# Optimization experiments

Hardware: AMD Instinct MI355X
Metric: run time of the kernel (lower is better)

## Reference

```python
import jax, jax.numpy as jnp
import numpy as np

N = 4096      # number of nodes
C = 8         # channels (w1..w8 in source)
IN_DIM = 256  # input feature dim
D = 64        # per-channel dim (c_dim)
OUT = 128     # out_dim
ITERS = 4     # routing iterations
BETA = 1.0    # temperature
DENSITY = 0.01


def _l2norm(x):
    # tf.nn.l2_normalize along last axis with eps=1e-12
    return x * jax.lax.rsqrt(jnp.maximum(jnp.sum(x * x, axis=-1, keepdims=True), 1e-12))


def setup_inputs() -> dict:
    key = jax.random.key(0)
    k0, k1, k2, k3, k4, k5 = jax.random.split(key, 6)
    features = jax.random.normal(k0, (N, IN_DIM), dtype=jnp.float32)
    # sparse-ish 0/1 adjacency stored densely (as in the original model)
    adj = (jax.random.uniform(k1, (N, N)) < DENSITY).astype(jnp.float32)
    W = jax.random.normal(k2, (C, IN_DIM, D), dtype=jnp.float32)    # w1..w8 stacked
    b = jax.random.normal(k3, (C, 1, D), dtype=jnp.float32)         # b1..b8 stacked
    W_o = jax.random.normal(k4, (C * D, OUT), dtype=jnp.float32)
    bias = jax.random.normal(k5, (1, OUT), dtype=jnp.float32)
    return {"features": features, "adj": adj, "W": W, "b": b, "W_o": W_o, "bias": bias}


def reference(features, adj, W, b, W_o, bias):
    mask = adj > 0  # [N, N]
    # per-channel projection + l2 normalize: z[c] = l2norm(features @ w[c] + b[c])
    z = _l2norm(jnp.einsum('ni,cid->cnd', features, W) + b)  # [C, N, D]
    for _ in range(ITERS):
        # dense per-channel attention (XX^T), masked by adjacency
        A = jnp.einsum('cnd,cmd->cnm', z, z)                 # [C, N, N]
        A = jnp.where(mask[None], A, 0.0) / BETA
        # softmax across channels at each (i, j), then re-mask
        A = jax.nn.softmax(A, axis=0)
        A = jnp.where(mask[None], A, 0.0)
        # aggregate + residual + l2 normalize
        z = _l2norm(z + jnp.einsum('cnm,cmd->cnd', A, z))
    # concat channels along feature axis: [N, C*D]
    h = jnp.transpose(z, (1, 0, 2)).reshape(N, C * D)
    # (dropout skipped: stochastic op, identity in the deterministic reference)
    return h @ W_o + bias
```

## Files before the change

kernel.cpp:

```cpp
#include <hip/hip_runtime.h>
#include <hip/hip_bf16.h>

#define N_NODES 4096
#define C_CH    8
#define IN_DIM  256
#define D_DIM   64
#define CD      512
#define OUT_DIM 128
#define ITERS   4
#define STRIDE  128

typedef __hip_bfloat16 bf16;
typedef short short8 __attribute__((ext_vector_type(8)));
typedef float floatx4 __attribute__((ext_vector_type(4)));

__device__ __forceinline__ float bf2f(bf16 x) { return __bfloat162float(x); }

__device__ __forceinline__ unsigned f2b_rne(float x) {
    unsigned u = __float_as_uint(x);
    return (u + 0x7FFFu + ((u >> 16) & 1u)) >> 16;
}
__device__ __forceinline__ unsigned pack2bf(float a, float b) {
    return f2b_rne(a) | (f2b_rne(b) << 16);
}
__device__ __forceinline__ void unpack2(unsigned v, float& a, float& b) {
    a = __uint_as_float(v << 16);
    b = __uint_as_float(v & 0xFFFF0000u);
}
__device__ __forceinline__ short8 as_s8(uint4 u) {
    union { uint4 a; short8 b; } x; x.a = u; return x.b;
}

__global__ void detect_kernel(const unsigned* __restrict__ feat_u,
                              int* __restrict__ flag) {
    int t = threadIdx.x;
    unsigned u = feat_u[t];
    int e = (u >> 7) & 0xFF;
    int vote = (e >= 0x68 && e <= 0x86) ? 1 : 0;
    __shared__ int sv[4];
    int lane = t & 63, wid = t >> 6;
    #pragma unroll
    for (int off = 32; off; off >>= 1) vote += __shfl_xor(vote, off);
    if (lane == 0) sv[wid] = vote;
    __syncthreads();
    if (t == 0) flag[0] = (sv[0] + sv[1] + sv[2] + sv[3] >= 128) ? 1 : 0;
}

__global__ void wflat_kernel(const void* __restrict__ W, float* __restrict__ Wflat,
                             const int* __restrict__ flag) {
    int idx = blockIdx.x * 256 + threadIdx.x;
    int d = idx & 63;
    int k = (idx >> 6) & 255;
    int c = idx >> 14;
    float v = (*flag) ? bf2f(((const bf16*)W)[idx]) : ((const float*)W)[idx];
    Wflat[k * CD + c * D_DIM + d] = v;
}

__global__ void wot_kernel(const void* __restrict__ Wo,
                           unsigned short* __restrict__ Wo_t,
                           const int* __restrict__ flag) {
    int idx = blockIdx.x * 256 + threadIdx.x;
    int k = idx >> 7, n = idx & 127;
    unsigned short v;
    if (*flag) v = ((const unsigned short*)Wo)[idx];
    else       v = (unsigned short)f2b_rne(((const float*)Wo)[idx]);
    Wo_t[n * CD + k] = v;
}

__global__ __launch_bounds__(256) void proj_kernel(
        const void* __restrict__ feat, const float* __restrict__ Wflat,
        const void* __restrict__ b, unsigned* __restrict__ zbf,
        const int* __restrict__ flag) {
    int nb = blockIdx.x * 8;
    int t  = threadIdx.x;
    __shared__ float fs[8 * IN_DIM];
    bool isbf = (*flag) != 0;

    if (isbf) {
        const uint4* p = (const uint4*)((const unsigned short*)feat + (size_t)nb * IN_DIM);
        uint4 u = p[t];
        float v[8];
        unpack2(u.x, v[0], v[1]); unpack2(u.y, v[2], v[3]);
        unpack2(u.z, v[4], v[5]); unpack2(u.w, v[6], v[7]);
        *(float4*)&fs[t * 8]     = make_float4(v[0], v[1], v[2], v[3]);
        *(float4*)&fs[t * 8 + 4] = make_float4(v[4], v[5], v[6], v[7]);
    } else {
        const float4* p = (const float4*)((const float*)feat + (size_t)nb * IN_DIM);
        float4 u0 = p[t];
        float4 u1 = p[t + 256];
        *(float4*)&fs[t * 4]         = u0;
        *(float4*)&fs[(t + 256) * 4] = u1;
    }
    __syncthreads();

    float a0[8] = {}, a1[8] = {};
    for (int k = 0; k < IN_DIM; k++) {
        float w0 = Wflat[k * CD + t];
        float w1 = Wflat[k * CD + 256 + t];
        #pragma unroll
        for (int r = 0; r < 8; r++) {
            float f = fs[r * IN_DIM + k];
            a0[r] = fmaf(f, w0, a0[r]);
            a1[r] = fmaf(f, w1, a1[r]);
        }
    }
    float b0 = isbf ? bf2f(((const bf16*)b)[t])       : ((const float*)b)[t];
    float b1 = isbf ? bf2f(((const bf16*)b)[256 + t]) : ((const float*)b)[256 + t];

    #pragma unroll
    for (int r = 0; r < 8; r++) {
        float v0 = a0[r] + b0;
        float v1 = a1[r] + b1;
        float ss0 = v0 * v0, ss1 = v1 * v1;
        #pragma unroll
        for (int off = 32; off; off >>= 1) {
            ss0 += __shfl_xor(ss0, off);
            ss1 += __shfl_xor(ss1, off);
        }
        float o0 = v0 * rsqrtf(fmaxf(ss0, 1e-12f));
        float o1 = v1 * rsqrtf(fmaxf(ss1, 1e-12f));
        size_t row = (size_t)(nb + r);
        float p0 = __shfl_xor(o0, 1);
        float p1 = __shfl_xor(o1, 1);
        if (!(t & 1)) {
            zbf[row * 256 + (t >> 1)]       = pack2bf(o0, p0);
            zbf[row * 256 + 128 + (t >> 1)] = pack2bf(o1, p1);
        }
    }
}

__global__ __launch_bounds__(256) void build_kernel(
        const void* __restrict__ adj, int* __restrict__ deg,
        int* __restrict__ col_buf, const int* __restrict__ flag) {
    int w = threadIdx.x >> 6, lane = threadIdx.x & 63;
    int i = blockIdx.x * 4 + w;
    bool isbf = (*flag) != 0;
    int base_out = i * STRIDE;
    int running = 0;
    int nch = isbf ? 8 : 16;

    for (int ch = 0; ch < nch; ch++) {
        unsigned bits = 0;
        int j0, nelem;
        if (isbf) {
            const uint4* p = (const uint4*)((const unsigned short*)adj + (size_t)i * N_NODES);
            uint4 u = p[ch * 64 + lane];
            j0 = (ch * 64 + lane) * 8; nelem = 8;
            unsigned short h[8] = {
                (unsigned short)(u.x & 0xFFFF), (unsigned short)(u.x >> 16),
                (unsigned short)(u.y & 0xFFFF), (unsigned short)(u.y >> 16),
                (unsigned short)(u.z & 0xFFFF), (unsigned short)(u.z >> 16),
                (unsigned short)(u.w & 0xFFFF), (unsigned short)(u.w >> 16)};
            #pragma unroll
            for (int k = 0; k < 8; k++)
                if ((h[k] & 0x8000) == 0 && h[k] != 0) bits |= (1u << k);
        } else {
            const float4* p = (const float4*)((const float*)adj + (size_t)i * N_NODES);
            float4 f = p[ch * 64 + lane];
            j0 = (ch * 64 + lane) * 4; nelem = 4;
            if (f.x > 0.f) bits |= 1u;
            if (f.y > 0.f) bits |= 2u;
            if (f.z > 0.f) bits |= 4u;
            if (f.w > 0.f) bits |= 8u;
        }
        int cnt = __popc(bits);
        int sc = cnt;
        #pragma unroll
        for (int off = 1; off < 64; off <<= 1) {
            int v = __shfl_up(sc, off);
            if (lane >= off) sc += v;
        }
        int tot = __shfl(sc, 63);
        int pos = base_out + running + (sc - cnt);
        for (int k = 0; k < nelem; k++) {
            if ((bits >> k) & 1u) {
                if (pos < base_out + STRIDE) col_buf[pos] = j0 + k;
                pos++;
            }
        }
        running += tot;
    }
    if (lane == 0) deg[i] = (running < STRIDE) ? running : STRIDE;
}

__device__ __forceinline__ void edge_step(const float zi[8], float acc[8], uint4 u) {
    float vj[8];
    unpack2(u.x, vj[0], vj[1]);
    unpack2(u.y, vj[2], vj[3]);
    unpack2(u.z, vj[4], vj[5]);
    unpack2(u.w, vj[6], vj[7]);
    float p = 0.f;
    #pragma unroll
    for (int k = 0; k < 8; k++) p = fmaf(zi[k], vj[k], p);
    p += __shfl_xor(p, 1); p += __shfl_xor(p, 2); p += __shfl_xor(p, 4);
    float ex = __expf(p);
    float s = ex;
    s += __shfl_xor(s, 8); s += __shfl_xor(s, 16); s += __shfl_xor(s, 32);
    float wgt = ex / s;
    #pragma unroll
    for (int k = 0; k < 8; k++) acc[k] = fmaf(wgt, vj[k], acc[k]);
}

__global__ __launch_bounds__(256) void route_kernel(
        const unsigned* __restrict__ zbf_in, unsigned* __restrict__ zbf_out,
        const int* __restrict__ deg, const int* __restrict__ col_buf) {
    int w = threadIdx.x >> 6, lane = threadIdx.x & 63;
    int pair = w >> 1;
    int half = w & 1;
    int i = blockIdx.x * 2 + pair;
    int g = lane >> 3, s = lane & 7;
    __shared__ int   s_cols[2][STRIDE];
    __shared__ float s_acc[2][CD];

    s_cols[pair][half * 64 + lane] = col_buf[i * STRIDE + half * 64 + lane];
    __syncthreads();

    int frag = g * 32 + s * 4;
    uint4 uown = *(const uint4*)(zbf_in + (size_t)i * 256 + frag);
    float zi[8], acc[8];
    unpack2(uown.x, zi[0], zi[1]); unpack2(uown.y, zi[2], zi[3]);
    unpack2(uown.z, zi[4], zi[5]); unpack2(uown.w, zi[6], zi[7]);
    #pragma unroll
    for (int k = 0; k < 8; k++) acc[k] = half ? 0.f : zi[k];

    int dg = deg[i];
    int e_mid = (dg + 1) >> 1;
    int e   = half ? e_mid : 0;
    int end = half ? dg    : e_mid;
    for (; e + 3 < end; e += 4) {
        int j0 = s_cols[pair][e]     & (N_NODES - 1);
        int j1 = s_cols[pair][e + 1] & (N_NODES - 1);
        int j2 = s_cols[pair][e + 2] & (N_NODES - 1);
        int j3 = s_cols[pair][e + 3] & (N_NODES - 1);
        uint4 u0 = *(const uint4*)(zbf_in + (size_t)j0 * 256 + frag);
        uint4 u1 = *(const uint4*)(zbf_in + (size_t)j1 * 256 + frag);
        uint4 u2 = *(const uint4*)(zbf_in + (size_t)j2 * 256 + frag);
        uint4 u3 = *(const uint4*)(zbf_in + (size_t)j3 * 256 + frag);
        edge_step(zi, acc, u0);
        edge_step(zi, acc, u1);
        edge_step(zi, acc, u2);
        edge_step(zi, acc, u3);
    }
    for (; e < end; e++) {
        int j0 = s_cols[pair][e] & (N_NODES - 1);
        uint4 u0 = *(const uint4*)(zbf_in + (size_t)j0 * 256 + frag);
        edge_step(zi, acc, u0);
    }

    int flat = g * D_DIM + s * 8;
    if (half) {
        *(float4*)&s_acc[pair][flat]     = make_float4(acc[0], acc[1], acc[2], acc[3]);
        *(float4*)&s_acc[pair][flat + 4] = make_float4(acc[4], acc[5], acc[6], acc[7]);
    }
    __syncthreads();
    if (!half) {
        float4 p0 = *(const float4*)&s_acc[pair][flat];
        float4 p1 = *(const float4*)&s_acc[pair][flat + 4];
        acc[0] += p0.x; acc[1] += p0.y; acc[2] += p0.z; acc[3] += p0.w;
        acc[4] += p1.x; acc[5] += p1.y; acc[6] += p1.z; acc[7] += p1.w;

        float ss = 0.f;
        #pragma unroll
        for (int k = 0; k < 8; k++) ss = fmaf(acc[k], acc[k], ss);
        ss += __shfl_xor(ss, 1); ss += __shfl_xor(ss, 2); ss += __shfl_xor(ss, 4);
        float sc = rsqrtf(fmaxf(ss, 1e-12f));
        float o[8];
        #pragma unroll
        for (int k = 0; k < 8; k++) o[k] = acc[k] * sc;

        uint4 ob;
        ob.x = pack2bf(o[0], o[1]); ob.y = pack2bf(o[2], o[3]);
        ob.z = pack2bf(o[4], o[5]); ob.w = pack2bf(o[6], o[7]);
        *(uint4*)(zbf_out + (size_t)i * 256 + frag) = ob;
    }
}

__global__ __launch_bounds__(256) void out_gemm_mfma(
        const unsigned* __restrict__ zbf, const unsigned* __restrict__ wot_u,
        const void* __restrict__ bias, void* __restrict__ out,
        const int* __restrict__ flag) {
    int w = threadIdx.x >> 6, lane = threadIdx.x & 63;
    int r0 = blockIdx.x * 32 + (w & 1) * 16;
    int n0 = (w >> 1) * 64;
    int m = lane & 15, quad = lane >> 4;

    floatx4 acc0 = {0.f, 0.f, 0.f, 0.f}, acc1 = acc0, acc2 = acc0, acc3 = acc0;
    const unsigned* ap  = zbf   + (size_t)(r0 + m) * 256 + quad * 4;
    const unsigned* bp0 = wot_u + (size_t)(n0 + m) * 256 + quad * 4;
    const unsigned* bp1 = bp0 + 16 * 256;
    const unsigned* bp2 = bp0 + 32 * 256;
    const unsigned* bp3 = bp0 + 48 * 256;

    #pragma unroll
    for (int k0 = 0; k0 < 256; k0 += 16) {
        short8 a  = as_s8(*(const uint4*)(ap  + k0));
        short8 b0 = as_s8(*(const uint4*)(bp0 + k0));
        short8 b1 = as_s8(*(const uint4*)(bp1 + k0));
        short8 b2 = as_s8(*(const uint4*)(bp2 + k0));
        short8 b3 = as_s8(*(const uint4*)(bp3 + k0));
        acc0 = __builtin_amdgcn_mfma_f32_16x16x32_bf16(a, b0, acc0, 0, 0, 0);
        acc1 = __builtin_amdgcn_mfma_f32_16x16x32_bf16(a, b1, acc1, 0, 0, 0);
        acc2 = __builtin_amdgcn_mfma_f32_16x16x32_bf16(a, b2, acc2, 0, 0, 0);
        acc3 = __builtin_amdgcn_mfma_f32_16x16x32_bf16(a, b3, acc3, 0, 0, 0);
    }

    bool isbf = (*flag) != 0;
    float accs[4][4] = {
        {acc0[0], acc0[1], acc0[2], acc0[3]},
        {acc1[0], acc1[1], acc1[2], acc1[3]},
        {acc2[0], acc2[1], acc2[2], acc2[3]},
        {acc3[0], acc3[1], acc3[2], acc3[3]}};
    #pragma unroll
    for (int c = 0; c < 4; c++) {
        int col = n0 + c * 16 + m;
        float bb = isbf ? bf2f(((const bf16*)bias)[col]) : ((const float*)bias)[col];
        #pragma unroll
        for (int r = 0; r < 4; r++) {
            int row = r0 + quad * 4 + r;
            float v = accs[c][r] + bb;
            size_t oi = (size_t)row * OUT_DIM + col;
            if (isbf) ((bf16*)out)[oi] = __float2bfloat16(v);
            else      ((float*)out)[oi] = v;
        }
    }
}

extern "C" void kernel_launch(void* const* d_in, const int* in_sizes, int n_in,
                              void* d_out, int out_size, void* d_ws, size_t ws_size,
                              hipStream_t stream) {
    const void* feat = d_in[0];
    const void* adj  = d_in[1];
    const void* W    = d_in[2];
    const void* b    = d_in[3];
    const void* Wo   = d_in[4];
    const void* bias = d_in[5];

    char* ws = (char*)d_ws;
    unsigned*       zbf_a = (unsigned*)ws;
    unsigned*       zbf_b = (unsigned*)(ws + (4u  << 20));
    unsigned short* Wo_t  = (unsigned short*)(ws + (8u << 20));
    float*          Wflat = (float*)(ws + (9u << 20));
    int*            flag  = (int*)  (ws + (10u << 20));
    int*            deg   = (int*)  (ws + (10u << 20) + (4u << 10));
    int*            col_buf = (int*)(ws + (11u << 20));

    detect_kernel<<<1, 256, 0, stream>>>((const unsigned*)feat, flag);
    wflat_kernel<<<(C_CH * IN_DIM * D_DIM) / 256, 256, 0, stream>>>(W, Wflat, flag);
    wot_kernel<<<(CD * OUT_DIM) / 256, 256, 0, stream>>>(Wo, Wo_t, flag);
    build_kernel<<<N_NODES / 4, 256, 0, stream>>>(adj, deg, col_buf, flag);
    proj_kernel<<<N_NODES / 8, 256, 0, stream>>>(feat, Wflat, b, zbf_a, flag);

    unsigned* bin = zbf_a;
    unsigned* bot = zbf_b;
    for (int it = 0; it < ITERS; it++) {
        route_kernel<<<N_NODES / 2, 256, 0, stream>>>(bin, bot, deg, col_buf);
        unsigned* tb = bin; bin = bot; bot = tb;
    }
    out_gemm_mfma<<<N_NODES / 32, 256, 0, stream>>>(bin, (const unsigned*)Wo_t, bias, d_out, flag);
}
```

Before: 248.7 us.

## Fuse preprocessing kernels and run routing iterations in one cooperative kernel

Merges the dtype detection, W flattening, Wo transpose, adjacency compaction and projection into a single heterogeneous launch, with each block inferring the dtype itself. The four routing iterations run in one cooperative kernel that separates them with grid-wide syncs, using one wave per node instead of splitting a node across two waves. The projection now reads W directly in its original layout instead of a pre-flattened copy, and the divide and rsqrt become fast hardware rcp/rsq. The aim is to cut launch overhead and the extra pass that materialised Wflat. In exchange, each wave walks the full edge list alone, so there is less parallelism per node, and grid sync has its own cost.

```diff
diff --git a/kernel.cpp b/kernel.cpp
--- a/kernel.cpp
+++ b/kernel.cpp
@@ -1,5 +1,8 @@
 #include <hip/hip_runtime.h>
 #include <hip/hip_bf16.h>
+#include <hip/hip_cooperative_groups.h>
+
+namespace cg = cooperative_groups;
 
 #define N_NODES 4096
 #define C_CH    8
@@ -31,156 +34,146 @@
     union { uint4 a; short8 b; } x; x.a = u; return x.b;
 }
 
-__global__ void detect_kernel(const unsigned* __restrict__ feat_u,
-                              int* __restrict__ flag) {
-    int t = threadIdx.x;
-    unsigned u = feat_u[t];
+__device__ __forceinline__ bool wave_detect(const unsigned* __restrict__ feat_u) {
+    int lane = threadIdx.x & 63;
+    unsigned u = feat_u[lane];
     int e = (u >> 7) & 0xFF;
     int vote = (e >= 0x68 && e <= 0x86) ? 1 : 0;
-    __shared__ int sv[4];
-    int lane = t & 63, wid = t >> 6;
     #pragma unroll
     for (int off = 32; off; off >>= 1) vote += __shfl_xor(vote, off);
-    if (lane == 0) sv[wid] = vote;
-    __syncthreads();
-    if (t == 0) flag[0] = (sv[0] + sv[1] + sv[2] + sv[3] >= 128) ? 1 : 0;
-}
-
-__global__ void wflat_kernel(const void* __restrict__ W, float* __restrict__ Wflat,
-                             const int* __restrict__ flag) {
-    int idx = blockIdx.x * 256 + threadIdx.x;
-    int d = idx & 63;
-    int k = (idx >> 6) & 255;
-    int c = idx >> 14;
-    float v = (*flag) ? bf2f(((const bf16*)W)[idx]) : ((const float*)W)[idx];
-    Wflat[k * CD + c * D_DIM + d] = v;
-}
-
-__global__ void wot_kernel(const void* __restrict__ Wo,
-                           unsigned short* __restrict__ Wo_t,
-                           const int* __restrict__ flag) {
-    int idx = blockIdx.x * 256 + threadIdx.x;
-    int k = idx >> 7, n = idx & 127;
-    unsigned short v;
-    if (*flag) v = ((const unsigned short*)Wo)[idx];
-    else       v = (unsigned short)f2b_rne(((const float*)Wo)[idx]);
-    Wo_t[n * CD + k] = v;
-}
-
-__global__ __launch_bounds__(256) void proj_kernel(
-        const void* __restrict__ feat, const float* __restrict__ Wflat,
-        const void* __restrict__ b, unsigned* __restrict__ zbf,
-        const int* __restrict__ flag) {
-    int nb = blockIdx.x * 8;
-    int t  = threadIdx.x;
-    __shared__ float fs[8 * IN_DIM];
-    bool isbf = (*flag) != 0;
-
-    if (isbf) {
-        const uint4* p = (const uint4*)((const unsigned short*)feat + (size_t)nb * IN_DIM);
-        uint4 u = p[t];
-        float v[8];
-        unpack2(u.x, v[0], v[1]); unpack2(u.y, v[2], v[3]);
-        unpack2(u.z, v[4], v[5]); unpack2(u.w, v[6], v[7]);
-        *(float4*)&fs[t * 8]     = make_float4(v[0], v[1], v[2], v[3]);
-        *(float4*)&fs[t * 8 + 4] = make_float4(v[4], v[5], v[6], v[7]);
+    return vote >= 32;
+}
+
+__global__ __launch_bounds__(256) void mega_pre(
+        const void* __restrict__ feat, const void* __restrict__ adj,
+        const void* __restrict__ W, const void* __restrict__ b,
+        const void* __restrict__ Wo,
+        unsigned* __restrict__ zbf, int* __restrict__ deg,
+        int* __restrict__ col_buf, unsigned short* __restrict__ Wo_t) {
+    bool isbf = wave_detect((const unsigned*)feat);
+    int bx = blockIdx.x;
+    int t = threadIdx.x;
+
+    if (bx < 512) {
+        int nb = bx * 8;
+        __shared__ float fs[8 * IN_DIM];
+        if (isbf) {
+            const uint4* p = (const uint4*)((const unsigned short*)feat + (size_t)nb * IN_DIM);
+            uint4 u = p[t];
+            float v[8];
+            unpack2(u.x, v[0], v[1]); unpack2(u.y, v[2], v[3]);
+            unpack2(u.z, v[4], v[5]); unpack2(u.w, v[6], v[7]);
+            *(float4*)&fs[t * 8]     = make_float4(v[0], v[1], v[2], v[3]);
+            *(float4*)&fs[t * 8 + 4] = make_float4(v[4], v[5], v[6], v[7]);
+        } else {
+            const float4* p = (const float4*)((const float*)feat + (size_t)nb * IN_DIM);
+            float4 u0 = p[t];
+            float4 u1 = p[t + 256];
+            *(float4*)&fs[t * 4]         = u0;
+            *(float4*)&fs[(t + 256) * 4] = u1;
+        }
+        __syncthreads();
+
+        int d = t & 63;
+        size_t wbase0 = (size_t)(t >> 6) * IN_DIM * D_DIM + d;
+        size_t wbase1 = (size_t)(4 + (t >> 6)) * IN_DIM * D_DIM + d;
+        float a0[8] = {}, a1[8] = {};
+        for (int k = 0; k < IN_DIM; k++) {
+            float w0, w1;
+            if (isbf) {
+                w0 = bf2f(((const bf16*)W)[wbase0 + k * D_DIM]);
+                w1 = bf2f(((const bf16*)W)[wbase1 + k * D_DIM]);
+            } else {
+                w0 = ((const float*)W)[wbase0 + k * D_DIM];
+                w1 = ((const float*)W)[wbase1 + k * D_DIM];
+            }
+            #pragma unroll
+            for (int r = 0; r < 8; r++) {
+                float f = fs[r * IN_DIM + k];
+                a0[r] = fmaf(f, w0, a0[r]);
+                a1[r] = fmaf(f, w1, a1[r]);
+            }
+        }
+        float b0 = isbf ? bf2f(((const bf16*)b)[t])       : ((const float*)b)[t];
+        float b1 = isbf ? bf2f(((const bf16*)b)[256 + t]) : ((const float*)b)[256 + t];
+
+        #pragma unroll
+        for (int r = 0; r < 8; r++) {
+            float v0 = a0[r] + b0;
+            float v1 = a1[r] + b1;
+            float ss0 = v0 * v0, ss1 = v1 * v1;
+            #pragma unroll
+            for (int off = 32; off; off >>= 1) {
+                ss0 += __shfl_xor(ss0, off);
+                ss1 += __shfl_xor(ss1, off);
+            }
+            float o0 = v0 * __builtin_amdgcn_rsqf(fmaxf(ss0, 1e-12f));
+            float o1 = v1 * __builtin_amdgcn_rsqf(fmaxf(ss1, 1e-12f));
+            size_t row = (size_t)(nb + r);
+            float p0 = __shfl_xor(o0, 1);
+            float p1 = __shfl_xor(o1, 1);
+            if (!(t & 1)) {
+                zbf[row * 256 + (t >> 1)]       = pack2bf(o0, p0);
+                zbf[row * 256 + 128 + (t >> 1)] = pack2bf(o1, p1);
+            }
+        }
+    } else if (bx < 1536) {
+        int w = t >> 6, lane = t & 63;
+        int i = (bx - 512) * 4 + w;
+        int base_out = i * STRIDE;
+        int running = 0;
+        int nch = isbf ? 8 : 16;
+        for (int ch = 0; ch < nch; ch++) {
+            unsigned bits = 0;
+            int j0, nelem;
+            if (isbf) {
+                const uint4* p = (const uint4*)((const unsigned short*)adj + (size_t)i * N_NODES);
+                uint4 u = p[ch * 64 + lane];
+                j0 = (ch * 64 + lane) * 8; nelem = 8;
+                unsigned short h[8] = {
+                    (unsigned short)(u.x & 0xFFFF), (unsigned short)(u.x >> 16),
+                    (unsigned short)(u.y & 0xFFFF), (unsigned short)(u.y >> 16),
+                    (unsigned short)(u.z & 0xFFFF), (unsigned short)(u.z >> 16),
+                    (unsigned short)(u.w & 0xFFFF), (unsigned short)(u.w >> 16)};
+                #pragma unroll
+                for (int k = 0; k < 8; k++)
+                    if ((h[k] & 0x8000) == 0 && h[k] != 0) bits |= (1u << k);
+            } else {
+                const float4* p = (const float4*)((const float*)adj + (size_t)i * N_NODES);
+                float4 f = p[ch * 64 + lane];
+                j0 = (ch * 64 + lane) * 4; nelem = 4;
+                if (f.x > 0.f) bits |= 1u;
+                if (f.y > 0.f) bits |= 2u;
+                if (f.z > 0.f) bits |= 4u;
+                if (f.w > 0.f) bits |= 8u;
+            }
+            int cnt = __popc(bits);
+            int sc = cnt;
+            #pragma unroll
+            for (int off = 1; off < 64; off <<= 1) {
+                int v = __shfl_up(sc, off);
+                if (lane >= off) sc += v;
+            }
+            int tot = __shfl(sc, 63);
+            int pos = base_out + running + (sc - cnt);
+            for (int k = 0; k < nelem; k++) {
+                if ((bits >> k) & 1u) {
+                    if (pos < base_out + STRIDE) col_buf[pos] = j0 + k;
+                    pos++;
+                }
+            }
+            running += tot;
+        }
+        if ((t & 63) == 0) deg[i] = (running < STRIDE) ? running : STRIDE;
     } else {
-        const float4* p = (const float4*)((const float*)feat + (size_t)nb * IN_DIM);
-        float4 u0 = p[t];
-        float4 u1 = p[t + 256];
-        *(float4*)&fs[t * 4]         = u0;
-        *(float4*)&fs[(t + 256) * 4] = u1;
+        int idx = (bx - 1536) * 256 + t;
+        int n = idx & 127;
+        int k = idx >> 7;
+        unsigned short v;
+        if (isbf) v = ((const unsigned short*)Wo)[idx];
+        else      v = (unsigned short)f2b_rne(((const float*)Wo)[idx]);
+        Wo_t[n * CD + k] = v;
     }
-    __syncthreads();
-
-    float a0[8] = {}, a1[8] = {};
-    for (int k = 0; k < IN_DIM; k++) {
-        float w0 = Wflat[k * CD + t];
-        float w1 = Wflat[k * CD + 256 + t];
-        #pragma unroll
-        for (int r = 0; r < 8; r++) {
-            float f = fs[r * IN_DIM + k];
-            a0[r] = fmaf(f, w0, a0[r]);
-            a1[r] = fmaf(f, w1, a1[r]);
-        }
-    }
-    float b0 = isbf ? bf2f(((const bf16*)b)[t])       : ((const float*)b)[t];
-    float b1 = isbf ? bf2f(((const bf16*)b)[256 + t]) : ((const float*)b)[256 + t];
-
-    #pragma unroll
-    for (int r = 0; r < 8; r++) {
-        float v0 = a0[r] + b0;
-        float v1 = a1[r] + b1;
-        float ss0 = v0 * v0, ss1 = v1 * v1;
-        #pragma unroll
-        for (int off = 32; off; off >>= 1) {
-            ss0 += __shfl_xor(ss0, off);
-            ss1 += __shfl_xor(ss1, off);
-        }
-        float o0 = v0 * rsqrtf(fmaxf(ss0, 1e-12f));
-        float o1 = v1 * rsqrtf(fmaxf(ss1, 1e-12f));
-        size_t row = (size_t)(nb + r);
-        float p0 = __shfl_xor(o0, 1);
-        float p1 = __shfl_xor(o1, 1);
-        if (!(t & 1)) {
-            zbf[row * 256 + (t >> 1)]       = pack2bf(o0, p0);
-            zbf[row * 256 + 128 + (t >> 1)] = pack2bf(o1, p1);
-        }
-    }
-}
-
-__global__ __launch_bounds__(256) void build_kernel(
-        const void* __restrict__ adj, int* __restrict__ deg,
-        int* __restrict__ col_buf, const int* __restrict__ flag) {
-    int w = threadIdx.x >> 6, lane = threadIdx.x & 63;
-    int i = blockIdx.x * 4 + w;
-    bool isbf = (*flag) != 0;
-    int base_out = i * STRIDE;
-    int running = 0;
-    int nch = isbf ? 8 : 16;
-
-    for (int ch = 0; ch < nch; ch++) {
-        unsigned bits = 0;
-        int j0, nelem;
-        if (isbf) {
-            const uint4* p = (const uint4*)((const unsigned short*)adj + (size_t)i * N_NODES);
-            uint4 u = p[ch * 64 + lane];
-            j0 = (ch * 64 + lane) * 8; nelem = 8;
-            unsigned short h[8] = {
-                (unsigned short)(u.x & 0xFFFF), (unsigned short)(u.x >> 16),
-                (unsigned short)(u.y & 0xFFFF), (unsigned short)(u.y >> 16),
-                (unsigned short)(u.z & 0xFFFF), (unsigned short)(u.z >> 16),
-                (unsigned short)(u.w & 0xFFFF), (unsigned short)(u.w >> 16)};
-            #pragma unroll
-            for (int k = 0; k < 8; k++)
-                if ((h[k] & 0x8000) == 0 && h[k] != 0) bits |= (1u << k);
-        } else {
-            const float4* p = (const float4*)((const float*)adj + (size_t)i * N_NODES);
-            float4 f = p[ch * 64 + lane];
-            j0 = (ch * 64 + lane) * 4; nelem = 4;
-            if (f.x > 0.f) bits |= 1u;
-            if (f.y > 0.f) bits |= 2u;
-            if (f.z > 0.f) bits |= 4u;
-            if (f.w > 0.f) bits |= 8u;
-        }
-        int cnt = __popc(bits);
-        int sc = cnt;
-        #pragma unroll
-        for (int off = 1; off < 64; off <<= 1) {
-            int v = __shfl_up(sc, off);
-            if (lane >= off) sc += v;
-        }
-        int tot = __shfl(sc, 63);
-        int pos = base_out + running + (sc - cnt);
-        for (int k = 0; k < nelem; k++) {
-            if ((bits >> k) & 1u) {
-                if (pos < base_out + STRIDE) col_buf[pos] = j0 + k;
-                pos++;
-            }
-        }
-        running += tot;
-    }
-    if (lane == 0) deg[i] = (running < STRIDE) ? running : STRIDE;
 }
 
 __device__ __forceinline__ void edge_step(const float zi[8], float acc[8], uint4 u) {
@@ -196,74 +189,61 @@
     float ex = __expf(p);
     float s = ex;
     s += __shfl_xor(s, 8); s += __shfl_xor(s, 16); s += __shfl_xor(s, 32);
-    float wgt = ex / s;
+    float wgt = ex * __builtin_amdgcn_rcpf(s);
     #pragma unroll
     for (int k = 0; k < 8; k++) acc[k] = fmaf(wgt, vj[k], acc[k]);
 }
 
-__global__ __launch_bounds__(256) void route_kernel(
-        const unsigned* __restrict__ zbf_in, unsigned* __restrict__ zbf_out,
+__global__ __launch_bounds__(256) void route_coop(
+        unsigned* __restrict__ zbf_a, unsigned* __restrict__ zbf_b,
         const int* __restrict__ deg, const int* __restrict__ col_buf) {
+    cg::grid_group gg = cg::this_grid();
     int w = threadIdx.x >> 6, lane = threadIdx.x & 63;
-    int pair = w >> 1;
-    int half = w & 1;
-    int i = blockIdx.x * 2 + pair;
+    int i = blockIdx.x * 4 + w;
     int g = lane >> 3, s = lane & 7;
-    __shared__ int   s_cols[2][STRIDE];
-    __shared__ float s_acc[2][CD];
-
-    s_cols[pair][half * 64 + lane] = col_buf[i * STRIDE + half * 64 + lane];
-    __syncthreads();
-
     int frag = g * 32 + s * 4;
-    uint4 uown = *(const uint4*)(zbf_in + (size_t)i * 256 + frag);
-    float zi[8], acc[8];
-    unpack2(uown.x, zi[0], zi[1]); unpack2(uown.y, zi[2], zi[3]);
-    unpack2(uown.z, zi[4], zi[5]); unpack2(uown.w, zi[6], zi[7]);
-    #pragma unroll
-    for (int k = 0; k < 8; k++) acc[k] = half ? 0.f : zi[k];
-
+
+    __shared__ int s_cols[4][STRIDE];
+    s_cols[w][lane]      = col_buf[i * STRIDE + lane];
+    s_cols[w][lane + 64] = col_buf[i * STRIDE + lane + 64];
     int dg = deg[i];
-    int e_mid = (dg + 1) >> 1;
-    int e   = half ? e_mid : 0;
-    int end = half ? dg    : e_mid;
-    for (; e + 3 < end; e += 4) {
-        int j0 = s_cols[pair][e]     & (N_NODES - 1);
-        int j1 = s_cols[pair][e + 1] & (N_NODES - 1);
-        int j2 = s_cols[pair][e + 2] & (N_NODES - 1);
-        int j3 = s_cols[pair][e + 3] & (N_NODES - 1);
-        uint4 u0 = *(const uint4*)(zbf_in + (size_t)j0 * 256 + frag);
-        uint4 u1 = *(const uint4*)(zbf_in + (size_t)j1 * 256 + frag);
-        uint4 u2 = *(const uint4*)(zbf_in + (size_t)j2 * 256 + frag);
-        uint4 u3 = *(const uint4*)(zbf_in + (size_t)j3 * 256 + frag);
-        edge_step(zi, acc, u0);
-        edge_step(zi, acc, u1);
-        edge_step(zi, acc, u2);
-        edge_step(zi, acc, u3);
-    }
-    for (; e < end; e++) {
-        int j0 = s_cols[pair][e] & (N_NODES - 1);
-        uint4 u0 = *(const uint4*)(zbf_in + (size_t)j0 * 256 + frag);
-        edge_step(zi, acc, u0);
-    }
-
-    int flat = g * D_DIM + s * 8;
-    if (half) {
-        *(float4*)&s_acc[pair][flat]     = make_float4(acc[0], acc[1], acc[2], acc[3]);
-        *(float4*)&s_acc[pair][flat + 4] = make_float4(acc[4], acc[5], acc[6], acc[7]);
-    }
-    __syncthreads();
-    if (!half) {
-        float4 p0 = *(const float4*)&s_acc[pair][flat];
-        float4 p1 = *(const float4*)&s_acc[pair][flat + 4];
-        acc[0] += p0.x; acc[1] += p0.y; acc[2] += p0.z; acc[3] += p0.w;
-        acc[4] += p1.x; acc[5] += p1.y; acc[6] += p1.z; acc[7] += p1.w;
+
+    const unsigned* in = zbf_a;
+    unsigned* out = zbf_b;
+    for (int it = 0; it < ITERS; it++) {
+        uint4 uown = *(const uint4*)(in + (size_t)i * 256 + frag);
+        float zi[8], acc[8];
+        unpack2(uown.x, zi[0], zi[1]); unpack2(uown.y, zi[2], zi[3]);
+        unpack2(uown.z, zi[4], zi[5]); unpack2(uown.w, zi[6], zi[7]);
+        #pragma unroll
+        for (int k = 0; k < 8; k++) acc[k] = zi[k];
+
+        int e = 0;
+        for (; e + 3 < dg; e += 4) {
+            int j0 = s_cols[w][e]     & (N_NODES - 1);
+            int j1 = s_cols[w][e + 1] & (N_NODES - 1);
+            int j2 = s_cols[w][e + 2] & (N_NODES - 1);
+            int j3 = s_cols[w][e + 3] & (N_NODES - 1);
+            uint4 u0 = *(const uint4*)(in + (size_t)j0 * 256 + frag);
+            uint4 u1 = *(const uint4*)(in + (size_t)j1 * 256 + frag);
+            uint4 u2 = *(const uint4*)(in + (size_t)j2 * 256 + frag);
+            uint4 u3 = *(const uint4*)(in + (size_t)j3 * 256 + frag);
+            edge_step(zi, acc, u0);
+            edge_step(zi, acc, u1);
+            edge_step(zi, acc, u2);
+            edge_step(zi, acc, u3);
+        }
+        for (; e < dg; e++) {
+            int j0 = s_cols[w][e] & (N_NODES - 1);
+            uint4 u0 = *(const uint4*)(in + (size_t)j0 * 256 + frag);
+            edge_step(zi, acc, u0);
+        }
 
         float ss = 0.f;
         #pragma unroll
         for (int k = 0; k < 8; k++) ss = fmaf(acc[k], acc[k], ss);
         ss += __shfl_xor(ss, 1); ss += __shfl_xor(ss, 2); ss += __shfl_xor(ss, 4);
-        float sc = rsqrtf(fmaxf(ss, 1e-12f));
+        float sc = __builtin_amdgcn_rsqf(fmaxf(ss, 1e-12f));
         float o[8];
         #pragma unroll
         for (int k = 0; k < 8; k++) o[k] = acc[k] * sc;
@@ -271,14 +251,18 @@
         uint4 ob;
         ob.x = pack2bf(o[0], o[1]); ob.y = pack2bf(o[2], o[3]);
         ob.z = pack2bf(o[4], o[5]); ob.w = pack2bf(o[6], o[7]);
-        *(uint4*)(zbf_out + (size_t)i * 256 + frag) = ob;
+        *(uint4*)(out + (size_t)i * 256 + frag) = ob;
+
+        if (it != ITERS - 1) gg.sync();
+        unsigned* tmp = (unsigned*)in; in = out; out = tmp;
     }
 }
 
 __global__ __launch_bounds__(256) void out_gemm_mfma(
         const unsigned* __restrict__ zbf, const unsigned* __restrict__ wot_u,
         const void* __restrict__ bias, void* __restrict__ out,
-        const int* __restrict__ flag) {
+        const void* __restrict__ feat) {
+    bool isbf = wave_detect((const unsigned*)feat);
     int w = threadIdx.x >> 6, lane = threadIdx.x & 63;
     int r0 = blockIdx.x * 32 + (w & 1) * 16;
     int n0 = (w >> 1) * 64;
@@ -304,7 +288,6 @@
         acc3 = __builtin_amdgcn_mfma_f32_16x16x32_bf16(a, b3, acc3, 0, 0, 0);
     }
 
-    bool isbf = (*flag) != 0;
     float accs[4][4] = {
         {acc0[0], acc0[1], acc0[2], acc0[3]},
         {acc1[0], acc1[1], acc1[2], acc1[3]},
@@ -336,25 +319,19 @@
     const void* bias = d_in[5];
 
     char* ws = (char*)d_ws;
-    unsigned*       zbf_a = (unsigned*)ws;
-    unsigned*       zbf_b = (unsigned*)(ws + (4u  << 20));
-    unsigned short* Wo_t  = (unsigned short*)(ws + (8u << 20));
-    float*          Wflat = (float*)(ws + (9u << 20));
-    int*            flag  = (int*)  (ws + (10u << 20));
-    int*            deg   = (int*)  (ws + (10u << 20) + (4u << 10));
-    int*            col_buf = (int*)(ws + (11u << 20));
-
-    detect_kernel<<<1, 256, 0, stream>>>((const unsigned*)feat, flag);
-    wflat_kernel<<<(C_CH * IN_DIM * D_DIM) / 256, 256, 0, stream>>>(W, Wflat, flag);
-    wot_kernel<<<(CD * OUT_DIM) / 256, 256, 0, stream>>>(Wo, Wo_t, flag);
-    build_kernel<<<N_NODES / 4, 256, 0, stream>>>(adj, deg, col_buf, flag);
-    proj_kernel<<<N_NODES / 8, 256, 0, stream>>>(feat, Wflat, b, zbf_a, flag);
-
-    unsigned* bin = zbf_a;
-    unsigned* bot = zbf_b;
-    for (int it = 0; it < ITERS; it++) {
-        route_kernel<<<N_NODES / 2, 256, 0, stream>>>(bin, bot, deg, col_buf);
-        unsigned* tb = bin; bin = bot; bot = tb;
-    }
-    out_gemm_mfma<<<N_NODES / 32, 256, 0, stream>>>(bin, (const unsigned*)Wo_t, bias, d_out, flag);
-}
+    unsigned*       zbf_a   = (unsigned*)ws;
+    unsigned*       zbf_b   = (unsigned*)(ws + (4u << 20));
+    unsigned short* Wo_t    = (unsigned short*)(ws + (8u << 20));
+    int*            deg     = (int*)(ws + (9u << 20));
+    int*            col_buf = (int*)(ws + (9u << 20) + (64u << 10));
+
+    mega_pre<<<1792, 256, 0, stream>>>(feat, adj, W, b, Wo,
+                                       zbf_a, deg, col_buf, Wo_t);
+
+    void* kargs[] = {(void*)&zbf_a, (void*)&zbf_b, (void*)&deg, (void*)&col_buf};
+    hipLaunchCooperativeKernel((void*)route_coop, dim3(1024), dim3(256),
+                               kargs, 0, stream);
+
+    out_gemm_mfma<<<N_NODES / 32, 256, 0, stream>>>(zbf_a, (const unsigned*)Wo_t,
+                                                    bias, d_out, feat);
+}
```

Result: slower. 609.2 us (+144.9%).
